# Kernel optimization log

Hardware: AMD Instinct MI355X
Metric: run time of the kernel (lower is better)

The kernel has to match this reference:

```python
import jax, jax.numpy as jnp
import numpy as np

BS, T, HS, WS = 2, 4, 32, 32
HW = HS * WS
D, NH, NL, NP = 256, 8, 4, 4
HD = D // NH
DFFN = 1024


def layer_norm(x, g, b, eps=1e-5):
    mu = jnp.mean(x, axis=-1, keepdims=True)
    var = jnp.mean((x - mu) ** 2, axis=-1, keepdims=True)
    return (x - mu) * jax.lax.rsqrt(var + eps) * g + b


def bilinear_gather(val, loc, Hl, Wl):
    # val: (bs, nh, Hl*Wl, hd); loc: (bs, Lq, nh, P, 2) in [0,1], last dim (x, y)
    # matches F.grid_sample(align_corners=False, padding_mode='zeros') on grid=2*loc-1
    x = loc[..., 0] * Wl - 0.5
    y = loc[..., 1] * Hl - 0.5
    x0 = jnp.floor(x)
    y0 = jnp.floor(y)
    lx = x - x0
    ly = y - y0
    bs, Lq, nh, P = x.shape
    out = jnp.zeros((bs, nh, Lq * P, val.shape[-1]), val.dtype)
    for dy in (0, 1):
        for dx in (0, 1):
            xi = x0 + dx
            yi = y0 + dy
            w = (lx if dx else 1.0 - lx) * (ly if dy else 1.0 - ly)
            valid = (xi >= 0) & (xi < Wl) & (yi >= 0) & (yi < Hl)
            w = jnp.where(valid, w, 0.0)
            xi_c = jnp.clip(xi, 0, Wl - 1).astype(jnp.int32)
            yi_c = jnp.clip(yi, 0, Hl - 1).astype(jnp.int32)
            idx = (yi_c * Wl + xi_c).transpose(0, 2, 1, 3).reshape(bs, nh, Lq * P)
            g = jnp.take_along_axis(val, idx[..., None], axis=2)
            wt = w.transpose(0, 2, 1, 3).reshape(bs, nh, Lq * P)
            out = out + wt[..., None] * g
    return out.reshape(bs, nh, Lq, P, val.shape[-1])


def setup_inputs() -> dict:
    key = jax.random.key(0)
    ks = jax.random.split(key, 12)
    s = 0.02
    return {
        "src": jax.random.normal(ks[0], (BS, T, HW, D), jnp.float32),
        "pos": jax.random.normal(ks[1], (BS, T, HW, D), jnp.float32),
        "reference_points": jax.random.uniform(ks[2], (BS, T * HW, NL, 2), jnp.float32),
        "value_proj_w": jax.random.normal(ks[3], (D, D), jnp.float32) * s,
        "value_proj_b": jnp.zeros((D,), jnp.float32),
        "sampling_offsets_w": jax.random.normal(ks[4], (D, NH * NL * NP * 2), jnp.float32) * s,
        "sampling_offsets_b": jax.random.normal(ks[5], (NH * NL * NP * 2,), jnp.float32) * s,
        "attn_weights_w": jax.random.normal(ks[6], (D, NH * NL * NP), jnp.float32) * s,
        "attn_weights_b": jnp.zeros((NH * NL * NP,), jnp.float32),
        "output_proj_w": jax.random.normal(ks[7], (D, D), jnp.float32) * s,
        "output_proj_b": jnp.zeros((D,), jnp.float32),
        "norm1_g": jnp.ones((D,), jnp.float32),
        "norm1_b": jnp.zeros((D,), jnp.float32),
        "linear1_w": jax.random.normal(ks[8], (D, DFFN), jnp.float32) * s,
        "linear1_b": jnp.zeros((DFFN,), jnp.float32),
        "linear2_w": jax.random.normal(ks[9], (DFFN, D), jnp.float32) * s,
        "linear2_b": jnp.zeros((D,), jnp.float32),
        "norm2_g": jnp.ones((D,), jnp.float32),
        "norm2_b": jnp.zeros((D,), jnp.float32),
        "spatial_shapes": np.array([[HS, WS]] * NL, np.int32),
        "level_start_index": np.arange(NL, dtype=np.int32) * HW,
    }


def reference(src, pos, reference_points, value_proj_w, value_proj_b,
              sampling_offsets_w, sampling_offsets_b, attn_weights_w, attn_weights_b,
              output_proj_w, output_proj_b, norm1_g, norm1_b,
              linear1_w, linear1_b, linear2_w, linear2_b, norm2_g, norm2_b,
              spatial_shapes, level_start_index):
    bs, t, hw, d = src.shape
    Lq = t * hw
    x = src.reshape(bs, Lq, d)
    q = x  # module never adds pos in forward (with_pos_embed unused)
    value = (x @ value_proj_w + value_proj_b).reshape(bs, Lq, NH, HD)
    offsets = (q @ sampling_offsets_w + sampling_offsets_b).reshape(bs, Lq, NH, NL, NP, 2)
    aw = jax.nn.softmax((q @ attn_weights_w + attn_weights_b).reshape(bs, Lq, NH, NL * NP), axis=-1)
    aw = aw.reshape(bs, Lq, NH, NL, NP)
    ss = np.asarray(spatial_shapes)
    lsi = np.asarray(level_start_index)
    offset_normalizer = jnp.asarray(ss[:, ::-1].copy(), src.dtype)  # (L, 2) = (W, H)
    sampling_locations = reference_points[:, :, None, :, None, :] + offsets / offset_normalizer[None, None, None, :, None, :]
    attn_out = jnp.zeros((bs, NH, Lq, HD), src.dtype)
    for l in range(NL):
        Hl, Wl = int(ss[l, 0]), int(ss[l, 1])
        start = int(lsi[l])
        v_l = value[:, start:start + Hl * Wl].transpose(0, 2, 1, 3)  # (bs, nh, HlWl, hd)
        samp = bilinear_gather(v_l, sampling_locations[:, :, :, l], Hl, Wl)  # (bs, nh, Lq, P, hd)
        w_l = aw[:, :, :, l].transpose(0, 2, 1, 3)  # (bs, nh, Lq, P)
        attn_out = attn_out + jnp.sum(samp * w_l[..., None], axis=3)
    attn_out = attn_out.transpose(0, 2, 1, 3).reshape(bs, Lq, d) @ output_proj_w + output_proj_b
    x = layer_norm(x + attn_out, norm1_g, norm1_b)
    ffn = jax.nn.relu(x @ linear1_w + linear1_b) @ linear2_w + linear2_b
    x = layer_norm(x + ffn, norm2_g, norm2_b)
    return x.reshape(bs, t, hw, d), sampling_locations
```

## Files before the change

kernel.cpp:

```cpp
#include <hip/hip_runtime.h>
#include <math.h>

#define ROWS   8192
#define LQ     4096
#define NHEAD  8
#define NLVL   4
#define NPTS   4
#define HDIM   32

typedef __attribute__((ext_vector_type(8))) short v8s;
typedef __attribute__((ext_vector_type(4))) float v4f;

__device__ __forceinline__ unsigned short f2bf(float x) {
    unsigned int u = __float_as_uint(x);
    u += 0x7fffu + ((u >> 16) & 1u);
    return (unsigned short)(u >> 16);
}
__device__ __forceinline__ float bf2f(unsigned short x) {
    return __uint_as_float(((unsigned int)x) << 16);
}

__global__ __launch_bounds__(256) void f2bf_k(const float* __restrict__ in,
                                              unsigned short* __restrict__ out, int n4)
{
    int i = blockIdx.x * 256 + threadIdx.x;
    if (i >= n4) return;
    float4 v = ((const float4*)in)[i];
    ushort4 o;
    o.x = f2bf(v.x); o.y = f2bf(v.y); o.z = f2bf(v.z); o.w = f2bf(v.w);
    ((ushort4*)out)[i] = o;
}

__global__ __launch_bounds__(256) void transT_k(const float* __restrict__ in,
                                                unsigned short* __restrict__ out,
                                                int K, int N, int ldout, int n_off)
{
    __shared__ float t[32][33];
    int tid = threadIdx.x;
    int tx = tid & 31, ty = tid >> 5;
    int k0 = blockIdx.y << 5, n0 = blockIdx.x << 5;
    #pragma unroll
    for (int i = 0; i < 4; i++)
        t[ty + i * 8][tx] = in[(size_t)(k0 + ty + i * 8) * N + n0 + tx];
    __syncthreads();
    #pragma unroll
    for (int i = 0; i < 4; i++)
        out[(size_t)(n_off + n0 + ty + i * 8) * ldout + k0 + tx] = f2bf(t[tx][ty + i * 8]);
}

__global__ __launch_bounds__(256) void biascat_k(const float* __restrict__ a,
                                                 const float* __restrict__ b,
                                                 const float* __restrict__ c,
                                                 float* __restrict__ out)
{
    int i = blockIdx.x * 256 + threadIdx.x;
    if (i < 256) out[i] = a[i];
    else if (i < 512) out[i] = b[i - 256];
    else if (i < 640) out[i] = c[i - 512];
}

template<bool PROJ, bool OUTBF, bool RELU, bool RES>
__global__ __launch_bounds__(256) void mfma_gemm_k(
    const unsigned short* __restrict__ A,
    const unsigned short* __restrict__ Bt,
    const float* __restrict__ bias,
    const float* __restrict__ res,
    void* __restrict__ Cout,
    unsigned short* __restrict__ vbf,
    int M, int N, int K)
{
    __shared__ __align__(16) unsigned short As[4][128][8];
    __shared__ __align__(16) unsigned short Bs[4][64][8];
    const int tid = threadIdx.x;
    const int row0 = blockIdx.y << 7, col0 = blockIdx.x << 6;
    const int wid = tid >> 6, lane = tid & 63;
    const int wm = wid & 1, wn = wid >> 1;
    const int lr = lane & 15, kq = lane >> 4;
    const int ar = tid >> 2, akq = tid & 3;
    const int bn = tid >> 2, bkq = tid & 3;

    v4f acc[4][2];
    #pragma unroll
    for (int i = 0; i < 4; i++)
        #pragma unroll
        for (int j = 0; j < 2; j++) acc[i][j] = (v4f){0.f, 0.f, 0.f, 0.f};

    for (int k0 = 0; k0 < K; k0 += 32) {
        float4 a0 = *(const float4*)(A + (size_t)(row0 + ar) * K + k0 + akq * 8);
        float4 a1 = *(const float4*)(A + (size_t)(row0 + ar + 64) * K + k0 + akq * 8);
        float4 b0 = *(const float4*)(Bt + (size_t)(col0 + bn) * K + k0 + bkq * 8);
        __syncthreads();
        *(float4*)(&As[akq][ar][0]) = a0;
        *(float4*)(&As[akq][ar + 64][0]) = a1;
        *(float4*)(&Bs[bkq][bn][0]) = b0;
        __syncthreads();
        v8s bf[2];
        #pragma unroll
        for (int nt = 0; nt < 2; nt++)
            bf[nt] = *(const v8s*)(&Bs[kq][wn * 32 + nt * 16 + lr][0]);
        #pragma unroll
        for (int mt = 0; mt < 4; mt++) {
            v8s af = *(const v8s*)(&As[kq][wm * 64 + mt * 16 + lr][0]);
            #pragma unroll
            for (int nt = 0; nt < 2; nt++)
                acc[mt][nt] = __builtin_amdgcn_mfma_f32_16x16x32_bf16(af, bf[nt], acc[mt][nt], 0, 0, 0);
        }
    }

    const int rq = lane >> 4;
    #pragma unroll
    for (int mt = 0; mt < 4; mt++) {
        #pragma unroll
        for (int nt = 0; nt < 2; nt++) {
            int col = col0 + wn * 32 + nt * 16 + lr;
            float bv = bias[col];
            #pragma unroll
            for (int i = 0; i < 4; i++) {
                int row = row0 + wm * 64 + mt * 16 + rq * 4 + i;
                float v = acc[mt][nt][i] + bv;
                if (RELU) v = fmaxf(v, 0.f);
                if (RES)  v += res[(size_t)row * N + col];
                if (PROJ) {
                    if (col0 < 256) {
                        int b = row >> 12, rb = row & 4095;
                        int l = rb >> 10, pix = rb & 1023;
                        int h = col >> 5, d = col & 31;
                        size_t idx = ((size_t)(((b << 2) + l) * 8 + h) << 15) + (pix << 5) + d;
                        vbf[idx] = f2bf(v);
                    } else {
                        ((float*)Cout)[(size_t)row * 384 + col - 256] = v;
                    }
                } else if (OUTBF) {
                    ((unsigned short*)Cout)[(size_t)row * N + col] = f2bf(v);
                } else {
                    ((float*)Cout)[(size_t)row * N + col] = v;
                }
            }
        }
    }
}

__global__ __launch_bounds__(256) void fused_gather_k(
    const float* __restrict__ po,
    const unsigned short* __restrict__ vbf,
    const float* __restrict__ refp,
    float* __restrict__ out_loc,
    unsigned short* __restrict__ attn_bf)
{
    int tid = threadIdx.x;
    int u = tid >> 5, l = (tid >> 3) & 3, d4 = tid & 7;
    int gid = blockIdx.x * 8 + u;
    int h = gid & 7, r = gid >> 3;
    int b = r >> 12;
    const float* prow = po + (size_t)r * 384;

    float2 rp = *(const float2*)(refp + (size_t)r * 8 + l * 2);

    float off[8];
    *(float4*)(off)     = *(const float4*)(prow + h * 32 + l * 8);
    *(float4*)(off + 4) = *(const float4*)(prow + h * 32 + l * 8 + 4);
    float locv[8];
    #pragma unroll
    for (int k = 0; k < 8; k++)
        locv[k] = ((k & 1) ? rp.y : rp.x) + off[k] * (1.f / 32.f);
    out_loc[(size_t)r * 256 + h * 32 + l * 8 + d4] = locv[d4];

    float w4[4];
    *(float4*)(w4) = *(const float4*)(prow + 256 + h * 16 + l * 4);
    float m = fmaxf(fmaxf(w4[0], w4[1]), fmaxf(w4[2], w4[3]));
    m = fmaxf(m, __shfl_xor(m, 8));
    m = fmaxf(m, __shfl_xor(m, 16));
    float s = 0.f;
    #pragma unroll
    for (int p = 0; p < 4; p++) { w4[p] = __expf(w4[p] - m); s += w4[p]; }
    s += __shfl_xor(s, 8);
    s += __shfl_xor(s, 16);
    float inv = 1.f / s;

    const unsigned short* vbase =
        vbf + (((size_t)(((b << 2) + l) * 8 + h)) << 15) + d4 * 4;
    ushort4 uv[16];
    float cw[16];
    #pragma unroll
    for (int p = 0; p < 4; p++) {
        float xf = locv[p * 2] * 32.f - 0.5f, yf = locv[p * 2 + 1] * 32.f - 0.5f;
        float x0f = floorf(xf), y0f = floorf(yf);
        float fx = xf - x0f, fy = yf - y0f;
        int x0 = (int)x0f, y0 = (int)y0f;
        float wgt = w4[p] * inv;
        #pragma unroll
        for (int dy = 0; dy < 2; dy++) {
            #pragma unroll
            for (int dx = 0; dx < 2; dx++) {
                int idx = p * 4 + dy * 2 + dx;
                int xi = x0 + dx, yi = y0 + dy;
                float wt = (dx ? fx : 1.f - fx) * (dy ? fy : 1.f - fy);
                bool valid = (xi >= 0) & (xi < 32) & (yi >= 0) & (yi < 32);
                int xc = min(max(xi, 0), 31), yc = min(max(yi, 0), 31);
                cw[idx] = valid ? (wgt * wt) : 0.f;
                uv[idx] = *(const ushort4*)(vbase + (size_t)((yc << 5) + xc) * 32);
            }
        }
    }
    float4 acc = {0.f, 0.f, 0.f, 0.f};
    #pragma unroll
    for (int idx = 0; idx < 16; idx++) {
        float c = cw[idx];
        acc.x += c * bf2f(uv[idx].x); acc.y += c * bf2f(uv[idx].y);
        acc.z += c * bf2f(uv[idx].z); acc.w += c * bf2f(uv[idx].w);
    }
    acc.x += __shfl_xor(acc.x, 8);  acc.y += __shfl_xor(acc.y, 8);
    acc.z += __shfl_xor(acc.z, 8);  acc.w += __shfl_xor(acc.w, 8);
    acc.x += __shfl_xor(acc.x, 16); acc.y += __shfl_xor(acc.y, 16);
    acc.z += __shfl_xor(acc.z, 16); acc.w += __shfl_xor(acc.w, 16);
    if (l == 0) {
        ushort4 o;
        o.x = f2bf(acc.x); o.y = f2bf(acc.y); o.z = f2bf(acc.z); o.w = f2bf(acc.w);
        *(ushort4*)(attn_bf + (size_t)r * 256 + h * 32 + d4 * 4) = o;
    }
}

template<bool WRITE_BF>
__global__ __launch_bounds__(256) void layernorm_k(
    float* __restrict__ x, const float* __restrict__ g, const float* __restrict__ b,
    unsigned short* __restrict__ xbf)
{
    int lane = threadIdx.x & 63;
    int wv = threadIdx.x >> 6;
    int row = blockIdx.x * 4 + wv;
    int c = lane << 2;
    float4 v = *(const float4*)(x + (size_t)row * 256 + c);
    float s = v.x + v.y + v.z + v.w;
    #pragma unroll
    for (int o = 1; o < 64; o <<= 1) s += __shfl_xor(s, o);
    float mu = s * (1.f / 256.f);
    float d0 = v.x - mu, d1 = v.y - mu, d2 = v.z - mu, d3 = v.w - mu;
    float vs = d0 * d0 + d1 * d1 + d2 * d2 + d3 * d3;
    #pragma unroll
    for (int o = 1; o < 64; o <<= 1) vs += __shfl_xor(vs, o);
    float rstd = rsqrtf(vs * (1.f / 256.f) + 1e-5f);
    float4 gg = *(const float4*)(g + c);
    float4 bb = *(const float4*)(b + c);
    float4 o4;
    o4.x = d0 * rstd * gg.x + bb.x;
    o4.y = d1 * rstd * gg.y + bb.y;
    o4.z = d2 * rstd * gg.z + bb.z;
    o4.w = d3 * rstd * gg.w + bb.w;
    *(float4*)(x + (size_t)row * 256 + c) = o4;
    if (WRITE_BF) {
        ushort4 ob;
        ob.x = f2bf(o4.x); ob.y = f2bf(o4.y); ob.z = f2bf(o4.z); ob.w = f2bf(o4.w);
        *(ushort4*)(xbf + (size_t)row * 256 + c) = ob;
    }
}

extern "C" void kernel_launch(void* const* d_in, const int* in_sizes, int n_in,
                              void* d_out, int out_size, void* d_ws, size_t ws_size,
                              hipStream_t stream)
{
    const float* src   = (const float*)d_in[0];
    const float* refp  = (const float*)d_in[2];
    const float* vw    = (const float*)d_in[3];
    const float* vb    = (const float*)d_in[4];
    const float* ofw   = (const float*)d_in[5];
    const float* ofb   = (const float*)d_in[6];
    const float* aww   = (const float*)d_in[7];
    const float* awb   = (const float*)d_in[8];
    const float* pw    = (const float*)d_in[9];
    const float* pb    = (const float*)d_in[10];
    const float* g1    = (const float*)d_in[11];
    const float* b1    = (const float*)d_in[12];
    const float* w1    = (const float*)d_in[13];
    const float* bi1   = (const float*)d_in[14];
    const float* w2    = (const float*)d_in[15];
    const float* bi2   = (const float*)d_in[16];
    const float* g2    = (const float*)d_in[17];
    const float* b2    = (const float*)d_in[18];

    float* ws = (float*)d_ws;
    float*          po        = ws;
    float*          x1        = ws + 3145728;
    unsigned short* value_bf  = (unsigned short*)(ws + 5242880);
    unsigned short* src_bf    = (unsigned short*)(ws + 6291456);
    unsigned short* x1_bf     = (unsigned short*)(ws + 7340032);
    unsigned short* attn_bf   = (unsigned short*)(ws + 8388608);
    unsigned short* hidden_bf = (unsigned short*)(ws + 9437184);
    unsigned short* Btcat     = (unsigned short*)(ws + 13631488);
    unsigned short* pwT       = (unsigned short*)(ws + 13713408);
    unsigned short* w1T       = (unsigned short*)(ws + 13746176);
    unsigned short* w2T       = (unsigned short*)(ws + 13877248);
    float*          biascat   = ws + 14008320;

    float* out_x   = (float*)d_out;
    float* out_loc = out_x + 2097152;

    dim3 blk(256);

    f2bf_k<<<2048, blk, 0, stream>>>(src, src_bf, 524288);
    transT_k<<<dim3(8, 8),  blk, 0, stream>>>(vw,  Btcat, 256, 256,  256, 0);
    transT_k<<<dim3(8, 8),  blk, 0, stream>>>(ofw, Btcat, 256, 256,  256, 256);
    transT_k<<<dim3(4, 8),  blk, 0, stream>>>(aww, Btcat, 256, 128,  256, 512);
    transT_k<<<dim3(8, 8),  blk, 0, stream>>>(pw,  pwT,   256, 256,  256, 0);
    transT_k<<<dim3(32, 8), blk, 0, stream>>>(w1,  w1T,   256, 1024, 256, 0);
    transT_k<<<dim3(8, 32), blk, 0, stream>>>(w2,  w2T,  1024, 256, 1024, 0);
    biascat_k<<<3, blk, 0, stream>>>(vb, ofb, awb, biascat);

    mfma_gemm_k<true, false, false, false><<<dim3(10, 64), blk, 0, stream>>>(
        src_bf, Btcat, biascat, nullptr, po, value_bf, ROWS, 640, 256);

    fused_gather_k<<<8192, blk, 0, stream>>>(po, value_bf, refp, out_loc, attn_bf);

    mfma_gemm_k<false, false, false, true><<<dim3(4, 64), blk, 0, stream>>>(
        attn_bf, pwT, pb, src, x1, nullptr, ROWS, 256, 256);
    layernorm_k<true><<<2048, blk, 0, stream>>>(x1, g1, b1, x1_bf);

    mfma_gemm_k<false, true, true, false><<<dim3(16, 64), blk, 0, stream>>>(
        x1_bf, w1T, bi1, nullptr, hidden_bf, nullptr, ROWS, 1024, 256);
    mfma_gemm_k<false, false, false, true><<<dim3(4, 64), blk, 0, stream>>>(
        hidden_bf, w2T, bi2, x1, out_x, nullptr, ROWS, 256, 1024);
    layernorm_k<false><<<2048, blk, 0, stream>>>(out_x, g2, b2, nullptr);
}
```

Baseline: 207.3 us.

## Merge prep kernels into one launch and load GEMM tiles directly to LDS

Eight small preprocessing launches (bf16 conversion of src, weight transposes, bias concat) are folded into a single prep kernel that dispatches on block index, cutting launch overhead. The GEMM staging now uses global_load_lds to copy A and B tiles straight into shared memory, skipping the register round trip. An XOR-style rotated k-chunk layout is meant to avoid LDS bank conflicts on the MFMA fragment reads. This depends on the direct-to-LDS builtin placing lanes contiguously, and the swizzle arithmetic adds address computation.

```diff
diff --git a/kernel.cpp b/kernel.cpp
--- a/kernel.cpp
+++ b/kernel.cpp
@@ -20,25 +20,20 @@
     return __uint_as_float(((unsigned int)x) << 16);
 }
 
-__global__ __launch_bounds__(256) void f2bf_k(const float* __restrict__ in,
-                                              unsigned short* __restrict__ out, int n4)
-{
-    int i = blockIdx.x * 256 + threadIdx.x;
-    if (i >= n4) return;
-    float4 v = ((const float4*)in)[i];
-    ushort4 o;
-    o.x = f2bf(v.x); o.y = f2bf(v.y); o.z = f2bf(v.z); o.w = f2bf(v.w);
-    ((ushort4*)out)[i] = o;
-}
-
-__global__ __launch_bounds__(256) void transT_k(const float* __restrict__ in,
-                                                unsigned short* __restrict__ out,
-                                                int K, int N, int ldout, int n_off)
+__device__ __forceinline__ void glds16(const void* g, void* l) {
+    __builtin_amdgcn_global_load_lds(
+        (const __attribute__((address_space(1))) unsigned int*)g,
+        (__attribute__((address_space(3))) unsigned int*)l, 16, 0, 0);
+}
+
+__device__ __forceinline__ void trans_tile(const float* __restrict__ in,
+                                           unsigned short* __restrict__ out,
+                                           int K, int N, int ldout, int n_off,
+                                           int bx, int by, int tid)
 {
     __shared__ float t[32][33];
-    int tid = threadIdx.x;
     int tx = tid & 31, ty = tid >> 5;
-    int k0 = blockIdx.y << 5, n0 = blockIdx.x << 5;
+    int k0 = by << 5, n0 = bx << 5;
     #pragma unroll
     for (int i = 0; i < 4; i++)
         t[ty + i * 8][tx] = in[(size_t)(k0 + ty + i * 8) * N + n0 + tx];
@@ -48,15 +43,40 @@
         out[(size_t)(n_off + n0 + ty + i * 8) * ldout + k0 + tx] = f2bf(t[tx][ty + i * 8]);
 }
 
-__global__ __launch_bounds__(256) void biascat_k(const float* __restrict__ a,
-                                                 const float* __restrict__ b,
-                                                 const float* __restrict__ c,
-                                                 float* __restrict__ out)
-{
-    int i = blockIdx.x * 256 + threadIdx.x;
-    if (i < 256) out[i] = a[i];
-    else if (i < 512) out[i] = b[i - 256];
-    else if (i < 640) out[i] = c[i - 512];
+__global__ __launch_bounds__(256) void prep_k(
+    const float* __restrict__ src, unsigned short* __restrict__ src_bf,
+    const float* __restrict__ vw, const float* __restrict__ ofw,
+    const float* __restrict__ aww, const float* __restrict__ pw,
+    const float* __restrict__ w1, const float* __restrict__ w2,
+    unsigned short* __restrict__ Btcat, unsigned short* __restrict__ pwT,
+    unsigned short* __restrict__ w1T, unsigned short* __restrict__ w2T,
+    const float* __restrict__ vb, const float* __restrict__ ofb,
+    const float* __restrict__ awb, float* __restrict__ biascat)
+{
+    int bid = blockIdx.x, tid = threadIdx.x;
+    if (bid < 2048) {
+        int i = bid * 256 + tid;
+        float4 v = ((const float4*)src)[i];
+        ushort4 o;
+        o.x = f2bf(v.x); o.y = f2bf(v.y); o.z = f2bf(v.z); o.w = f2bf(v.w);
+        ((ushort4*)src_bf)[i] = o;
+    } else if (bid < 2112) {
+        int t = bid - 2048; trans_tile(vw, Btcat, 256, 256, 256, 0, t & 7, t >> 3, tid);
+    } else if (bid < 2176) {
+        int t = bid - 2112; trans_tile(ofw, Btcat, 256, 256, 256, 256, t & 7, t >> 3, tid);
+    } else if (bid < 2208) {
+        int t = bid - 2176; trans_tile(aww, Btcat, 256, 128, 256, 512, t & 3, t >> 2, tid);
+    } else if (bid < 2272) {
+        int t = bid - 2208; trans_tile(pw, pwT, 256, 256, 256, 0, t & 7, t >> 3, tid);
+    } else if (bid < 2528) {
+        int t = bid - 2272; trans_tile(w1, w1T, 256, 1024, 256, 0, t & 31, t >> 5, tid);
+    } else if (bid < 2784) {
+        int t = bid - 2528; trans_tile(w2, w2T, 1024, 256, 1024, 0, t & 7, t >> 3, tid);
+    } else {
+        biascat[tid] = vb[tid];
+        biascat[tid + 256] = ofb[tid];
+        if (tid < 128) biascat[tid + 512] = awb[tid];
+    }
 }
 
 template<bool PROJ, bool OUTBF, bool RELU, bool RES>
@@ -69,15 +89,13 @@
     unsigned short* __restrict__ vbf,
     int M, int N, int K)
 {
-    __shared__ __align__(16) unsigned short As[4][128][8];
-    __shared__ __align__(16) unsigned short Bs[4][64][8];
+    __shared__ __align__(16) unsigned short As[4096];
+    __shared__ __align__(16) unsigned short Bs[2048];
     const int tid = threadIdx.x;
     const int row0 = blockIdx.y << 7, col0 = blockIdx.x << 6;
     const int wid = tid >> 6, lane = tid & 63;
     const int wm = wid & 1, wn = wid >> 1;
     const int lr = lane & 15, kq = lane >> 4;
-    const int ar = tid >> 2, akq = tid & 3;
-    const int bn = tid >> 2, bkq = tid & 3;
 
     v4f acc[4][2];
     #pragma unroll
@@ -86,21 +104,35 @@
         for (int j = 0; j < 2; j++) acc[i][j] = (v4f){0.f, 0.f, 0.f, 0.f};
 
     for (int k0 = 0; k0 < K; k0 += 32) {
-        float4 a0 = *(const float4*)(A + (size_t)(row0 + ar) * K + k0 + akq * 8);
-        float4 a1 = *(const float4*)(A + (size_t)(row0 + ar + 64) * K + k0 + akq * 8);
-        float4 b0 = *(const float4*)(Bt + (size_t)(col0 + bn) * K + k0 + bkq * 8);
         __syncthreads();
-        *(float4*)(&As[akq][ar][0]) = a0;
-        *(float4*)(&As[akq][ar + 64][0]) = a1;
-        *(float4*)(&Bs[bkq][bn][0]) = b0;
+        #pragma unroll
+        for (int i = 0; i < 2; i++) {
+            int c = wid * 128 + i * 64 + lane;
+            int row = c >> 2;
+            int kk = ((c & 3) + (row >> 2)) & 3;
+            glds16(A + (size_t)(row0 + row) * K + k0 + kk * 8,
+                   &As[(wid * 128 + i * 64) * 8]);
+        }
+        {
+            int c = wid * 64 + lane;
+            int row = c >> 2;
+            int kk = ((c & 3) + (row >> 2)) & 3;
+            glds16(Bt + (size_t)(col0 + row) * K + k0 + kk * 8,
+                   &Bs[wid * 512]);
+        }
         __syncthreads();
         v8s bf[2];
         #pragma unroll
-        for (int nt = 0; nt < 2; nt++)
-            bf[nt] = *(const v8s*)(&Bs[kq][wn * 32 + nt * 16 + lr][0]);
+        for (int nt = 0; nt < 2; nt++) {
+            int row = wn * 32 + nt * 16 + lr;
+            int s = (kq - (row >> 2)) & 3;
+            bf[nt] = *(const v8s*)(&Bs[(row * 4 + s) * 8]);
+        }
         #pragma unroll
         for (int mt = 0; mt < 4; mt++) {
-            v8s af = *(const v8s*)(&As[kq][wm * 64 + mt * 16 + lr][0]);
+            int row = wm * 64 + mt * 16 + lr;
+            int s = (kq - (row >> 2)) & 3;
+            v8s af = *(const v8s*)(&As[(row * 4 + s) * 8]);
             #pragma unroll
             for (int nt = 0; nt < 2; nt++)
                 acc[mt][nt] = __builtin_amdgcn_mfma_f32_16x16x32_bf16(af, bf[nt], acc[mt][nt], 0, 0, 0);
@@ -296,14 +328,8 @@
 
     dim3 blk(256);
 
-    f2bf_k<<<2048, blk, 0, stream>>>(src, src_bf, 524288);
-    transT_k<<<dim3(8, 8),  blk, 0, stream>>>(vw,  Btcat, 256, 256,  256, 0);
-    transT_k<<<dim3(8, 8),  blk, 0, stream>>>(ofw, Btcat, 256, 256,  256, 256);
-    transT_k<<<dim3(4, 8),  blk, 0, stream>>>(aww, Btcat, 256, 128,  256, 512);
-    transT_k<<<dim3(8, 8),  blk, 0, stream>>>(pw,  pwT,   256, 256,  256, 0);
-    transT_k<<<dim3(32, 8), blk, 0, stream>>>(w1,  w1T,   256, 1024, 256, 0);
-    transT_k<<<dim3(8, 32), blk, 0, stream>>>(w2,  w2T,  1024, 256, 1024, 0);
-    biascat_k<<<3, blk, 0, stream>>>(vb, ofb, awb, biascat);
+    prep_k<<<2785, blk, 0, stream>>>(src, src_bf, vw, ofw, aww, pw, w1, w2,
+                                     Btcat, pwT, w1T, w2T, vb, ofb, awb, biascat);
 
     mfma_gemm_k<true, false, false, false><<<dim3(10, 64), blk, 0, stream>>>(
         src_bf, Btcat, biascat, nullptr, po, value_bf, ROWS, 640, 256);
```

Measured after the change: 191.1 us. 1.08x faster.
